# Performance work log

Hardware: AMD Instinct MI355X
Metric: run time of the kernel (lower is better)

Reference implementation:

```python
import jax, jax.numpy as jnp
import numpy as np

N_NODES = 100000
N_EDGES = 1_600_000


def setup_inputs() -> dict:
    key = jax.random.key(0)
    ks = jax.random.split(key, 18)
    glorot = lambda k, fi, fo: jax.random.normal(k, (fi, fo), jnp.float32) * np.sqrt(2.0 / (fi + fo))
    inp = {
        "x": jax.random.normal(ks[0], (N_NODES, 5), jnp.float32),
        "edge_index": jax.random.randint(ks[1], (2, N_EDGES), 0, N_NODES, jnp.int64 if jax.config.jax_enable_x64 else jnp.int32),
        "W1": glorot(ks[2], 5, 32),  "b1": jnp.zeros((32,), jnp.float32),
        "W2": glorot(ks[3], 32, 32), "b2": jnp.zeros((32,), jnp.float32),
        "W3": glorot(ks[4], 32, 32), "b3": jnp.zeros((32,), jnp.float32),
        "Wd": glorot(ks[5], 32, 1),  "bd": jnp.zeros((1,), jnp.float32),
        "Wa": glorot(ks[6], 32, 1),  "ba": jnp.zeros((1,), jnp.float32),
        "Wt": glorot(ks[7], 32, 2),  "bt": jnp.zeros((2,), jnp.float32),
        "Wact": glorot(ks[8], 32, 9), "bact": jnp.zeros((9,), jnp.float32),
    }
    return inp


def _gcn_layer(x, row, col, norm, W, b):
    # GCNConv(add_self_loops=False): out[col] += norm * (x @ W)[row], then + bias
    h = x @ W                                  # [N, F_out]
    msg = h[row] * norm[:, None]               # [E, F_out]
    return jax.ops.segment_sum(msg, col, num_segments=N_NODES) + b


def reference(x, edge_index, W1, b1, W2, b2, W3, b3, Wd, bd, Wa, ba, Wt, bt, Wact, bact):
    row, col = edge_index[0], edge_index[1]
    # symmetric gcn normalization: deg over targets (unit edge weights)
    deg = jax.ops.segment_sum(jnp.ones((row.shape[0],), x.dtype), col, num_segments=N_NODES)
    dis = jnp.where(deg > 0, jax.lax.rsqrt(jnp.maximum(deg, 1.0)), 0.0)
    norm = dis[row] * dis[col]                 # [E]

    h = jax.nn.relu(_gcn_layer(x, row, col, norm, W1, b1))   # dropout = identity (eval)
    h = jax.nn.relu(_gcn_layer(h, row, col, norm, W2, b2))
    h = jax.nn.relu(_gcn_layer(h, row, col, norm, W3, b3))

    distance_scores = (h @ Wd + bd)[:, 0]      # [N]
    attention_scores = (h @ Wa + ba)[:, 0]     # [N]
    target_idx = jnp.argmax(attention_scores)
    h_t = h[target_idx]                        # [32]
    target_location_score = h_t @ Wt + bt      # [2]
    action_logits = h_t @ Wact + bact          # [9]
    return distance_scores, attention_scores, target_location_score, action_logits
```

## Files before the change

kernel.cpp:

```cpp
#include <hip/hip_runtime.h>
#include <hip/hip_fp16.h>
#include <math.h>

#define N_NODES 100000
#define F 32
#define BUCKET 64
#define NB ((N_NODES + BUCKET - 1) / BUCKET)
#define NBLK 128
#define SMAX 1536

__global__ void hist_kernel(const int* __restrict__ col, int* __restrict__ counts, int E) {
    __shared__ int hist[NB];
    int tid = threadIdx.x, blk = blockIdx.x;
    for (int i = tid; i < NB; i += 256) hist[i] = 0;
    __syncthreads();
    int chunk = (E + NBLK - 1) / NBLK;
    int beg = blk * chunk;
    int end = beg + chunk; if (end > E) end = E;
    for (int e = beg + tid; e < end; e += 256) atomicAdd(&hist[col[e] >> 6], 1);
    __syncthreads();
    for (int i = tid; i < NB; i += 256) counts[(size_t)blk * NB + i] = hist[i];
}

__global__ void offA_kernel(const int* __restrict__ counts, int* __restrict__ bucket_base,
                            int* __restrict__ rowstart, int E) {
    __shared__ int tot[NB];
    __shared__ int psum[1024];
    int tid = threadIdx.x;
    for (int b = tid; b < NB; b += 1024) {
        int s = 0;
        for (int blk = 0; blk < NBLK; blk++) s += counts[(size_t)blk * NB + b];
        tot[b] = s;
    }
    __syncthreads();
    int b0 = 2 * tid, b1 = 2 * tid + 1;
    int t0 = (b0 < NB) ? tot[b0] : 0;
    int t1 = (b1 < NB) ? tot[b1] : 0;
    int s = t0 + t1;
    psum[tid] = s;
    __syncthreads();
    for (int off = 1; off < 1024; off <<= 1) {
        int v = (tid >= off) ? psum[tid - off] : 0;
        __syncthreads();
        psum[tid] += v;
        __syncthreads();
    }
    int excl = psum[tid] - s;
    if (b0 < NB) bucket_base[b0] = excl;
    if (b1 < NB) bucket_base[b1] = excl + t0;
    if (tid == 1023) { bucket_base[NB] = psum[1023]; rowstart[N_NODES] = psum[1023]; }
}

__global__ void offB_kernel(const int* __restrict__ counts, const int* __restrict__ bucket_base,
                            int* __restrict__ boff) {
    int b = blockIdx.x * 256 + threadIdx.x;
    if (b >= NB) return;
    int running = bucket_base[b];
    for (int blk = 0; blk < NBLK; blk++) {
        boff[(size_t)blk * NB + b] = running;
        running += counts[(size_t)blk * NB + b];
    }
}

__global__ void scatter_kernel(const int* __restrict__ row, const int* __restrict__ col,
                               const int* __restrict__ boff, unsigned* __restrict__ storage, int E) {
    __shared__ int cur[NB];
    int tid = threadIdx.x, blk = blockIdx.x;
    for (int i = tid; i < NB; i += 256) cur[i] = boff[(size_t)blk * NB + i];
    __syncthreads();
    int chunk = (E + NBLK - 1) / NBLK;
    int beg = blk * chunk;
    int end = beg + chunk; if (end > E) end = E;
    for (int e = beg + tid; e < end; e += 256) {
        int c = col[e], r = row[e];
        int pos = atomicAdd(&cur[c >> 6], 1);
        storage[pos] = ((unsigned)(c & 63) << 17) | (unsigned)r;
    }
}

__global__ void csr_build_kernel(const unsigned* __restrict__ storage, const int* __restrict__ bucket_base,
                                 int* __restrict__ rowstart, int* __restrict__ csr_src,
                                 float* __restrict__ dis, const float* __restrict__ x,
                                 float* __restrict__ xd, int n) {
    __shared__ unsigned sh[SMAX];
    __shared__ int outloc[SMAX];
    __shared__ int hist[BUCKET];
    __shared__ int pre[BUCKET];
    __shared__ int cur[BUCKET];
    __shared__ float dloc[BUCKET];
    int b = blockIdx.x, tid = threadIdx.x;
    if (tid < BUCKET) hist[tid] = 0;
    __syncthreads();
    int base = bucket_base[b];
    int tot = bucket_base[b + 1] - base;
    if (tot > SMAX) tot = SMAX;
    for (int i = tid; i < tot; i += 256) sh[i] = storage[base + i];
    __syncthreads();
    for (int i = tid; i < tot; i += 256) atomicAdd(&hist[sh[i] >> 17], 1);
    __syncthreads();
    if (tid < BUCKET) pre[tid] = hist[tid];
    __syncthreads();
    for (int off = 1; off < BUCKET; off <<= 1) {
        int v = 0;
        if (tid < BUCKET && tid >= off) v = pre[tid - off];
        __syncthreads();
        if (tid < BUCKET && tid >= off) pre[tid] += v;
        __syncthreads();
    }
    if (tid < BUCKET) {
        int excl = pre[tid] - hist[tid];
        cur[tid] = excl;
        int node = b * BUCKET + tid;
        if (node < n) {
            rowstart[node] = base + excl;
            int d = hist[tid];
            float dv = (d > 0) ? rsqrtf((float)d) : 0.0f;
            dis[node] = dv;
            dloc[tid] = dv;
        }
    }
    __syncthreads();
    for (int i = tid; i < BUCKET * 8; i += 256) {
        int nl = i >> 3, f = i & 7;
        int node = b * BUCKET + nl;
        if (node < n) xd[(size_t)node * 8 + f] = (f < 5) ? dloc[nl] * x[(size_t)node * 5 + f] : 0.0f;
    }
    for (int i = tid; i < tot; i += 256) {
        unsigned p = sh[i];
        int pos = atomicAdd(&cur[p >> 17], 1);
        outloc[pos] = (int)(p & 0x1FFFF);
    }
    __syncthreads();
    for (int i = tid; i < tot; i += 256) csr_src[base + i] = outloc[i];
}

__global__ void gather8_kernel(const float* __restrict__ xd, const int* __restrict__ rowstart,
                               const int* __restrict__ csr_src, float* __restrict__ s1, int n) {
    int tid = threadIdx.x;
    int node = blockIdx.x * 32 + (tid >> 3);
    if (node >= n) return;
    int f = tid & 7;
    int start = rowstart[node], end = rowstart[node + 1];
    float a0 = 0, a1 = 0, a2 = 0, a3 = 0, a4 = 0, a5 = 0, a6 = 0, a7 = 0;
    int i = start;
    for (; i + 7 < end; i += 8) {
        int r0 = csr_src[i], r1 = csr_src[i+1], r2 = csr_src[i+2], r3 = csr_src[i+3];
        int r4 = csr_src[i+4], r5 = csr_src[i+5], r6 = csr_src[i+6], r7 = csr_src[i+7];
        a0 += xd[r0*8+f]; a1 += xd[r1*8+f]; a2 += xd[r2*8+f]; a3 += xd[r3*8+f];
        a4 += xd[r4*8+f]; a5 += xd[r5*8+f]; a6 += xd[r6*8+f]; a7 += xd[r7*8+f];
    }
    for (; i < end; i++) a0 += xd[csr_src[i]*8+f];
    s1[node*8+f] = ((a0+a1)+(a2+a3)) + ((a4+a5)+(a6+a7));
}

__global__ void pt1_kernel(const float* __restrict__ s1, const float* __restrict__ dis,
                           const float* __restrict__ W1, const float* __restrict__ b1,
                           __half* __restrict__ gdh, int n) {
    __shared__ float Ws[5 * F];
    int tid = threadIdx.x;
    if (tid < 5 * F) Ws[tid] = W1[tid];
    __syncthreads();
    int node = blockIdx.x * 8 + (tid >> 5);
    if (node >= n) return;
    int f = tid & 31;
    float dv = dis[node];
    float acc = b1[f];
#pragma unroll
    for (int k = 0; k < 5; k++) acc += dv * s1[node*8+k] * Ws[k*F+f];
    float h = acc > 0.0f ? acc : 0.0f;
    gdh[(size_t)node*F+f] = __float2half(dv * h);
}

__global__ void layer_mid_fused(const __half2* __restrict__ gin, const int* __restrict__ rowstart,
                                const int* __restrict__ csr_src, const float* __restrict__ dis,
                                const float* __restrict__ W, const float* __restrict__ bb,
                                __half2* __restrict__ gout, int n) {
    __shared__ float Ws[F * F];
    __shared__ float hs[16][F + 1];
    int tid = threadIdx.x;
    for (int i = tid; i < F * F; i += 256) Ws[i] = W[i];
    int grp = tid >> 4;
    int l2 = tid & 15;
    int node = blockIdx.x * 16 + grp;
    float dv = 0.0f;
    if (node < n) {
        int start = rowstart[node], end = rowstart[node + 1];
        float x0=0,y0=0,x1=0,y1=0,x2=0,y2=0,x3=0,y3=0;
        float x4=0,y4=0,x5=0,y5=0,x6=0,y6=0,x7=0,y7=0;
        int i = start;
        for (; i + 7 < end; i += 8) {
            int r0 = csr_src[i],   r1 = csr_src[i+1], r2 = csr_src[i+2], r3 = csr_src[i+3];
            int r4 = csr_src[i+4], r5 = csr_src[i+5], r6 = csr_src[i+6], r7 = csr_src[i+7];
            float2 f0 = __half22float2(gin[(size_t)r0*16 + l2]);
            float2 f1 = __half22float2(gin[(size_t)r1*16 + l2]);
            float2 f2 = __half22float2(gin[(size_t)r2*16 + l2]);
            float2 f3 = __half22float2(gin[(size_t)r3*16 + l2]);
            float2 f4 = __half22float2(gin[(size_t)r4*16 + l2]);
            float2 f5 = __half22float2(gin[(size_t)r5*16 + l2]);
            float2 f6 = __half22float2(gin[(size_t)r6*16 + l2]);
            float2 f7 = __half22float2(gin[(size_t)r7*16 + l2]);
            x0+=f0.x; y0+=f0.y; x1+=f1.x; y1+=f1.y; x2+=f2.x; y2+=f2.y; x3+=f3.x; y3+=f3.y;
            x4+=f4.x; y4+=f4.y; x5+=f5.x; y5+=f5.y; x6+=f6.x; y6+=f6.y; x7+=f7.x; y7+=f7.y;
        }
        for (; i < end; i++) {
            float2 fv = __half22float2(gin[(size_t)csr_src[i]*16 + l2]);
            x0 += fv.x; y0 += fv.y;
        }
        dv = dis[node];
        hs[grp][2*l2]   = dv * (((x0+x1)+(x2+x3)) + ((x4+x5)+(x6+x7)));
        hs[grp][2*l2+1] = dv * (((y0+y1)+(y2+y3)) + ((y4+y5)+(y6+y7)));
    }
    __syncthreads();
    if (node < n) {
        int fx = 2*l2, fy = 2*l2+1;
        float accx = bb[fx], accy = bb[fy];
#pragma unroll
        for (int k = 0; k < F; k++) {
            float hv = hs[grp][k];
            accx += hv * Ws[k*F+fx];
            accy += hv * Ws[k*F+fy];
        }
        float hx = accx > 0.0f ? accx : 0.0f;
        float hy = accy > 0.0f ? accy : 0.0f;
        gout[(size_t)node*16 + l2] = __floats2half2_rn(dv * hx, dv * hy);
    }
}

__global__ void layer_last_fused(const __half2* __restrict__ gin, const int* __restrict__ rowstart,
                                 const int* __restrict__ csr_src, const float* __restrict__ dis,
                                 const float* __restrict__ W3, const float* __restrict__ b3,
                                 const float* __restrict__ Wd, const float* __restrict__ bd,
                                 const float* __restrict__ Wa, const float* __restrict__ ba,
                                 float* __restrict__ out, float* __restrict__ pmax,
                                 int* __restrict__ pidx, int n) {
    __shared__ float Ws[F * F];
    __shared__ float hs[16][F + 1];
    __shared__ float gmax[16];
    __shared__ int gidx[16];
    int tid = threadIdx.x;
    for (int i = tid; i < F * F; i += 256) Ws[i] = W3[i];
    int grp = tid >> 4;
    int l2 = tid & 15;
    int node = blockIdx.x * 16 + grp;
    float dv = 0.0f;
    if (node < n) {
        int start = rowstart[node], end = rowstart[node + 1];
        float x0=0,y0=0,x1=0,y1=0,x2=0,y2=0,x3=0,y3=0;
        float x4=0,y4=0,x5=0,y5=0,x6=0,y6=0,x7=0,y7=0;
        int i = start;
        for (; i + 7 < end; i += 8) {
            int r0 = csr_src[i],   r1 = csr_src[i+1], r2 = csr_src[i+2], r3 = csr_src[i+3];
            int r4 = csr_src[i+4], r5 = csr_src[i+5], r6 = csr_src[i+6], r7 = csr_src[i+7];
            float2 f0 = __half22float2(gin[(size_t)r0*16 + l2]);
            float2 f1 = __half22float2(gin[(size_t)r1*16 + l2]);
            float2 f2 = __half22float2(gin[(size_t)r2*16 + l2]);
            float2 f3 = __half22float2(gin[(size_t)r3*16 + l2]);
            float2 f4 = __half22float2(gin[(size_t)r4*16 + l2]);
            float2 f5 = __half22float2(gin[(size_t)r5*16 + l2]);
            float2 f6 = __half22float2(gin[(size_t)r6*16 + l2]);
            float2 f7 = __half22float2(gin[(size_t)r7*16 + l2]);
            x0+=f0.x; y0+=f0.y; x1+=f1.x; y1+=f1.y; x2+=f2.x; y2+=f2.y; x3+=f3.x; y3+=f3.y;
            x4+=f4.x; y4+=f4.y; x5+=f5.x; y5+=f5.y; x6+=f6.x; y6+=f6.y; x7+=f7.x; y7+=f7.y;
        }
        for (; i < end; i++) {
            float2 fv = __half22float2(gin[(size_t)csr_src[i]*16 + l2]);
            x0 += fv.x; y0 += fv.y;
        }
        dv = dis[node];
        hs[grp][2*l2]   = dv * (((x0+x1)+(x2+x3)) + ((x4+x5)+(x6+x7)));
        hs[grp][2*l2+1] = dv * (((y0+y1)+(y2+y3)) + ((y4+y5)+(y6+y7)));
    }
    __syncthreads();
    if (node < n) {
        int fx = 2*l2, fy = 2*l2+1;
        float accx = b3[fx], accy = b3[fy];
#pragma unroll
        for (int k = 0; k < F; k++) {
            float hv = hs[grp][k];
            accx += hv * Ws[k*F+fx];
            accy += hv * Ws[k*F+fy];
        }
        float hx = accx > 0.0f ? accx : 0.0f;
        float hy = accy > 0.0f ? accy : 0.0f;
        float dterm = hx * Wd[fx] + hy * Wd[fy];
        float aterm = hx * Wa[fx] + hy * Wa[fy];
#pragma unroll
        for (int off = 8; off > 0; off >>= 1) {
            dterm += __shfl_xor(dterm, off);
            aterm += __shfl_xor(aterm, off);
        }
        if (l2 == 0) {
            out[node] = dterm + bd[0];
            float asc = aterm + ba[0];
            out[N_NODES + node] = asc;
            gmax[grp] = asc;
            gidx[grp] = node;
        }
    } else if (l2 == 0) {
        gmax[grp] = -INFINITY;
        gidx[grp] = 0x7fffffff;
    }
    __syncthreads();
    if (tid == 0) {
        float best = gmax[0]; int bi = gidx[0];
        for (int g = 1; g < 16; g++) {
            if (gmax[g] > best || (gmax[g] == best && gidx[g] < bi)) { best = gmax[g]; bi = gidx[g]; }
        }
        pmax[blockIdx.x] = best;
        pidx[blockIdx.x] = bi;
    }
}

__global__ void final_kernel(const float* __restrict__ pmax, const int* __restrict__ pidx, int nblocks,
                             const __half* __restrict__ gin, const int* __restrict__ rowstart,
                             const int* __restrict__ csr_src, const float* __restrict__ dis,
                             const float* __restrict__ W3, const float* __restrict__ b3,
                             const float* __restrict__ Wt, const float* __restrict__ bt,
                             const float* __restrict__ Wact, const float* __restrict__ bact,
                             float* __restrict__ out) {
    __shared__ float smax[256];
    __shared__ int sidx[256];
    __shared__ float part[8][F];
    __shared__ float hrow[F];
    __shared__ float ht[F];
    int tid = threadIdx.x;
    float best = -INFINITY; int bi = 0x7fffffff;
    for (int i = tid; i < nblocks; i += 256) {
        float v = pmax[i]; int ix = pidx[i];
        if (v > best || (v == best && ix < bi)) { best = v; bi = ix; }
    }
    smax[tid] = best; sidx[tid] = bi;
    __syncthreads();
    for (int st = 128; st > 0; st >>= 1) {
        if (tid < st) {
            float v2 = smax[tid + st]; int i2 = sidx[tid + st];
            if (v2 > smax[tid] || (v2 == smax[tid] && i2 < sidx[tid])) { smax[tid] = v2; sidx[tid] = i2; }
        }
        __syncthreads();
    }
    int target = sidx[0];
    int g = tid >> 5, f = tid & 31;
    int start = rowstart[target], end = rowstart[target + 1];
    float acc = 0.0f;
    for (int i = start + g; i < end; i += 8)
        acc += __half2float(gin[(size_t)csr_src[i] * F + f]);
    part[g][f] = acc;
    __syncthreads();
    if (tid < F) {
        float s = 0.0f;
#pragma unroll
        for (int gg = 0; gg < 8; gg++) s += part[gg][tid];
        hrow[tid] = dis[target] * s;
    }
    __syncthreads();
    if (tid < F) {
        float a = b3[tid];
#pragma unroll
        for (int k = 0; k < F; k++) a += hrow[k] * W3[k*F+tid];
        ht[tid] = a > 0.0f ? a : 0.0f;
    }
    __syncthreads();
    if (tid < 2) {
        float a = bt[tid];
#pragma unroll
        for (int k = 0; k < F; k++) a += ht[k] * Wt[k*2+tid];
        out[2 * N_NODES + tid] = a;
    } else if (tid < 11) {
        int j = tid - 2;
        float a = bact[j];
#pragma unroll
        for (int k = 0; k < F; k++) a += ht[k] * Wact[k*9+j];
        out[2 * N_NODES + 2 + j] = a;
    }
}

extern "C" void kernel_launch(void* const* d_in, const int* in_sizes, int n_in,
                              void* d_out, int out_size, void* d_ws, size_t ws_size,
                              hipStream_t stream) {
    const float* x  = (const float*)d_in[0];
    const int*   ei = (const int*)d_in[1];
    const int E = in_sizes[1] / 2;
    const int* row = ei;
    const int* col = ei + E;
    const float* W1 = (const float*)d_in[2];
    const float* b1 = (const float*)d_in[3];
    const float* W2 = (const float*)d_in[4];
    const float* b2 = (const float*)d_in[5];
    const float* W3 = (const float*)d_in[6];
    const float* b3 = (const float*)d_in[7];
    const float* Wd = (const float*)d_in[8];
    const float* bd = (const float*)d_in[9];
    const float* Wa = (const float*)d_in[10];
    const float* ba = (const float*)d_in[11];
    const float* Wt = (const float*)d_in[12];
    const float* bt = (const float*)d_in[13];
    const float* Wact = (const float*)d_in[14];
    const float* bact = (const float*)d_in[15];

    float* out = (float*)d_out;
    float* ws  = (float*)d_ws;

    float*    dis      = ws;
    float*    xd       = ws + N_NODES;
    float*    s1       = ws + (size_t)9 * N_NODES;
    __half*   gd_a     = (__half*)(ws + (size_t)17 * N_NODES);
    __half*   gd_b     = (__half*)(ws + (size_t)33 * N_NODES);
    unsigned* storage  = (unsigned*)(ws + (size_t)33 * N_NODES);
    int*      bucket_base = (int*)(ws + (size_t)49 * N_NODES);
    int*      counts   = bucket_base + NB + 1;
    int*      boff     = counts + NBLK * NB;
    int*      rowstart = boff + NBLK * NB;
    int*      csr_src  = rowstart + N_NODES + 1;
    float*    pmax     = (float*)(csr_src + E);
    int*      pidx     = (int*)(pmax + 12500);

    const int B = 256;
    const int nb16 = (N_NODES + 15) / 16;

    hist_kernel<<<NBLK, B, 0, stream>>>(col, counts, E);
    offA_kernel<<<1, 1024, 0, stream>>>(counts, bucket_base, rowstart, E);
    offB_kernel<<<(NB + 255) / 256, B, 0, stream>>>(counts, bucket_base, boff);
    scatter_kernel<<<NBLK, B, 0, stream>>>(row, col, boff, storage, E);
    csr_build_kernel<<<NB, B, 0, stream>>>(storage, bucket_base, rowstart, csr_src, dis, x, xd, N_NODES);

    gather8_kernel<<<(N_NODES + 31) / 32, B, 0, stream>>>(xd, rowstart, csr_src, s1, N_NODES);
    pt1_kernel<<<(N_NODES + 7) / 8, B, 0, stream>>>(s1, dis, W1, b1, gd_a, N_NODES);

    layer_mid_fused<<<nb16, B, 0, stream>>>((const __half2*)gd_a, rowstart, csr_src, dis,
                                            W2, b2, (__half2*)gd_b, N_NODES);

    layer_last_fused<<<nb16, B, 0, stream>>>((const __half2*)gd_b, rowstart, csr_src, dis,
                                             W3, b3, Wd, bd, Wa, ba, out, pmax, pidx, N_NODES);
    final_kernel<<<1, B, 0, stream>>>(pmax, pidx, nb16, gd_b, rowstart, csr_src, dis,
                                      W3, b3, Wt, bt, Wact, bact, out);
}
```

Baseline: 279.5 us.

## Fuse layer-1 gather with transform, parallelize bucket totals, deepen gather unroll

Merges the layer-1 neighbour gather and the 5→32 transform into one kernel, so the s1 intermediate is no longer written to and read back from global memory, and one launch is dropped. The per-bucket total reduction moves out of the single-block offset kernel into a multi-block kernel, which removes a serial bottleneck at the cost of one extra launch. The mid and last layer gathers now issue 16 independent index and feature loads per iteration to raise memory-level parallelism, which costs more registers and could lower occupancy.

```diff
diff --git a/kernel.cpp b/kernel.cpp
--- a/kernel.cpp
+++ b/kernel.cpp
@@ -22,17 +22,18 @@
     for (int i = tid; i < NB; i += 256) counts[(size_t)blk * NB + i] = hist[i];
 }
 
-__global__ void offA_kernel(const int* __restrict__ counts, int* __restrict__ bucket_base,
-                            int* __restrict__ rowstart, int E) {
-    __shared__ int tot[NB];
+__global__ void tot_kernel(const int* __restrict__ counts, int* __restrict__ tot) {
+    int b = blockIdx.x * 256 + threadIdx.x;
+    if (b >= NB) return;
+    int s = 0;
+    for (int blk = 0; blk < NBLK; blk++) s += counts[(size_t)blk * NB + b];
+    tot[b] = s;
+}
+
+__global__ void offA_kernel(const int* __restrict__ tot, int* __restrict__ bucket_base,
+                            int* __restrict__ rowstart) {
     __shared__ int psum[1024];
     int tid = threadIdx.x;
-    for (int b = tid; b < NB; b += 1024) {
-        int s = 0;
-        for (int blk = 0; blk < NBLK; blk++) s += counts[(size_t)blk * NB + b];
-        tot[b] = s;
-    }
-    __syncthreads();
     int b0 = 2 * tid, b1 = 2 * tid + 1;
     int t0 = (b0 < NB) ? tot[b0] : 0;
     int t1 = (b1 < NB) ? tot[b1] : 0;
@@ -134,41 +135,46 @@
     for (int i = tid; i < tot; i += 256) csr_src[base + i] = outloc[i];
 }
 
-__global__ void gather8_kernel(const float* __restrict__ xd, const int* __restrict__ rowstart,
-                               const int* __restrict__ csr_src, float* __restrict__ s1, int n) {
-    int tid = threadIdx.x;
-    int node = blockIdx.x * 32 + (tid >> 3);
-    if (node >= n) return;
-    int f = tid & 7;
-    int start = rowstart[node], end = rowstart[node + 1];
-    float a0 = 0, a1 = 0, a2 = 0, a3 = 0, a4 = 0, a5 = 0, a6 = 0, a7 = 0;
-    int i = start;
-    for (; i + 7 < end; i += 8) {
-        int r0 = csr_src[i], r1 = csr_src[i+1], r2 = csr_src[i+2], r3 = csr_src[i+3];
-        int r4 = csr_src[i+4], r5 = csr_src[i+5], r6 = csr_src[i+6], r7 = csr_src[i+7];
-        a0 += xd[r0*8+f]; a1 += xd[r1*8+f]; a2 += xd[r2*8+f]; a3 += xd[r3*8+f];
-        a4 += xd[r4*8+f]; a5 += xd[r5*8+f]; a6 += xd[r6*8+f]; a7 += xd[r7*8+f];
-    }
-    for (; i < end; i++) a0 += xd[csr_src[i]*8+f];
-    s1[node*8+f] = ((a0+a1)+(a2+a3)) + ((a4+a5)+(a6+a7));
-}
-
-__global__ void pt1_kernel(const float* __restrict__ s1, const float* __restrict__ dis,
-                           const float* __restrict__ W1, const float* __restrict__ b1,
-                           __half* __restrict__ gdh, int n) {
+__global__ void layer1_fused(const float* __restrict__ xd, const int* __restrict__ rowstart,
+                             const int* __restrict__ csr_src, const float* __restrict__ dis,
+                             const float* __restrict__ W1, const float* __restrict__ b1,
+                             __half* __restrict__ gda, int n) {
     __shared__ float Ws[5 * F];
+    __shared__ float s1s[32][8];
     int tid = threadIdx.x;
     if (tid < 5 * F) Ws[tid] = W1[tid];
-    __syncthreads();
-    int node = blockIdx.x * 8 + (tid >> 5);
-    if (node >= n) return;
-    int f = tid & 31;
-    float dv = dis[node];
-    float acc = b1[f];
-#pragma unroll
-    for (int k = 0; k < 5; k++) acc += dv * s1[node*8+k] * Ws[k*F+f];
-    float h = acc > 0.0f ? acc : 0.0f;
-    gdh[(size_t)node*F+f] = __float2half(dv * h);
+    int grp = tid >> 3, f = tid & 7;
+    int node = blockIdx.x * 32 + grp;
+    float sum = 0.0f;
+    if (node < n) {
+        int start = rowstart[node], end = rowstart[node + 1];
+        float a0 = 0, a1 = 0, a2 = 0, a3 = 0, a4 = 0, a5 = 0, a6 = 0, a7 = 0;
+        int i = start;
+        for (; i + 7 < end; i += 8) {
+            int r0 = csr_src[i], r1 = csr_src[i+1], r2 = csr_src[i+2], r3 = csr_src[i+3];
+            int r4 = csr_src[i+4], r5 = csr_src[i+5], r6 = csr_src[i+6], r7 = csr_src[i+7];
+            a0 += xd[r0*8+f]; a1 += xd[r1*8+f]; a2 += xd[r2*8+f]; a3 += xd[r3*8+f];
+            a4 += xd[r4*8+f]; a5 += xd[r5*8+f]; a6 += xd[r6*8+f]; a7 += xd[r7*8+f];
+        }
+        for (; i < end; i++) a0 += xd[csr_src[i]*8+f];
+        sum = ((a0+a1)+(a2+a3)) + ((a4+a5)+(a6+a7));
+    }
+    s1s[grp][f] = sum;
+    __syncthreads();
+    if (node < n) {
+        float dv = dis[node];
+        float sk0 = dv * s1s[grp][0], sk1 = dv * s1s[grp][1], sk2 = dv * s1s[grp][2];
+        float sk3 = dv * s1s[grp][3], sk4 = dv * s1s[grp][4];
+        int fb = f * 4;
+#pragma unroll
+        for (int j = 0; j < 4; j++) {
+            int ff = fb + j;
+            float acc = b1[ff] + sk0 * Ws[0*F+ff] + sk1 * Ws[1*F+ff] + sk2 * Ws[2*F+ff]
+                       + sk3 * Ws[3*F+ff] + sk4 * Ws[4*F+ff];
+            float h = acc > 0.0f ? acc : 0.0f;
+            gda[(size_t)node * F + ff] = __float2half(dv * h);
+        }
+    }
 }
 
 __global__ void layer_mid_fused(const __half2* __restrict__ gin, const int* __restrict__ rowstart,
@@ -185,30 +191,41 @@
     float dv = 0.0f;
     if (node < n) {
         int start = rowstart[node], end = rowstart[node + 1];
-        float x0=0,y0=0,x1=0,y1=0,x2=0,y2=0,x3=0,y3=0;
-        float x4=0,y4=0,x5=0,y5=0,x6=0,y6=0,x7=0,y7=0;
+        float accx[4] = {0,0,0,0}, accy[4] = {0,0,0,0};
         int i = start;
+        for (; i + 15 < end; i += 16) {
+            int r[16];
+#pragma unroll
+            for (int j = 0; j < 16; j++) r[j] = csr_src[i + j];
+            __half2 hv[16];
+#pragma unroll
+            for (int j = 0; j < 16; j++) hv[j] = gin[(size_t)r[j] * 16 + l2];
+#pragma unroll
+            for (int j = 0; j < 16; j++) {
+                float2 fv = __half22float2(hv[j]);
+                accx[j & 3] += fv.x; accy[j & 3] += fv.y;
+            }
+        }
         for (; i + 7 < end; i += 8) {
-            int r0 = csr_src[i],   r1 = csr_src[i+1], r2 = csr_src[i+2], r3 = csr_src[i+3];
-            int r4 = csr_src[i+4], r5 = csr_src[i+5], r6 = csr_src[i+6], r7 = csr_src[i+7];
-            float2 f0 = __half22float2(gin[(size_t)r0*16 + l2]);
-            float2 f1 = __half22float2(gin[(size_t)r1*16 + l2]);
-            float2 f2 = __half22float2(gin[(size_t)r2*16 + l2]);
-            float2 f3 = __half22float2(gin[(size_t)r3*16 + l2]);
-            float2 f4 = __half22float2(gin[(size_t)r4*16 + l2]);
-            float2 f5 = __half22float2(gin[(size_t)r5*16 + l2]);
-            float2 f6 = __half22float2(gin[(size_t)r6*16 + l2]);
-            float2 f7 = __half22float2(gin[(size_t)r7*16 + l2]);
-            x0+=f0.x; y0+=f0.y; x1+=f1.x; y1+=f1.y; x2+=f2.x; y2+=f2.y; x3+=f3.x; y3+=f3.y;
-            x4+=f4.x; y4+=f4.y; x5+=f5.x; y5+=f5.y; x6+=f6.x; y6+=f6.y; x7+=f7.x; y7+=f7.y;
+            int r[8];
+#pragma unroll
+            for (int j = 0; j < 8; j++) r[j] = csr_src[i + j];
+            __half2 hv[8];
+#pragma unroll
+            for (int j = 0; j < 8; j++) hv[j] = gin[(size_t)r[j] * 16 + l2];
+#pragma unroll
+            for (int j = 0; j < 8; j++) {
+                float2 fv = __half22float2(hv[j]);
+                accx[j & 3] += fv.x; accy[j & 3] += fv.y;
+            }
         }
         for (; i < end; i++) {
-            float2 fv = __half22float2(gin[(size_t)csr_src[i]*16 + l2]);
-            x0 += fv.x; y0 += fv.y;
+            float2 fv = __half22float2(gin[(size_t)csr_src[i] * 16 + l2]);
+            accx[0] += fv.x; accy[0] += fv.y;
         }
         dv = dis[node];
-        hs[grp][2*l2]   = dv * (((x0+x1)+(x2+x3)) + ((x4+x5)+(x6+x7)));
-        hs[grp][2*l2+1] = dv * (((y0+y1)+(y2+y3)) + ((y4+y5)+(y6+y7)));
+        hs[grp][2*l2]   = dv * ((accx[0]+accx[1]) + (accx[2]+accx[3]));
+        hs[grp][2*l2+1] = dv * ((accy[0]+accy[1]) + (accy[2]+accy[3]));
     }
     __syncthreads();
     if (node < n) {
@@ -245,30 +262,41 @@
     float dv = 0.0f;
     if (node < n) {
         int start = rowstart[node], end = rowstart[node + 1];
-        float x0=0,y0=0,x1=0,y1=0,x2=0,y2=0,x3=0,y3=0;
-        float x4=0,y4=0,x5=0,y5=0,x6=0,y6=0,x7=0,y7=0;
+        float accx[4] = {0,0,0,0}, accy[4] = {0,0,0,0};
         int i = start;
+        for (; i + 15 < end; i += 16) {
+            int r[16];
+#pragma unroll
+            for (int j = 0; j < 16; j++) r[j] = csr_src[i + j];
+            __half2 hv[16];
+#pragma unroll
+            for (int j = 0; j < 16; j++) hv[j] = gin[(size_t)r[j] * 16 + l2];
+#pragma unroll
+            for (int j = 0; j < 16; j++) {
+                float2 fv = __half22float2(hv[j]);
+                accx[j & 3] += fv.x; accy[j & 3] += fv.y;
+            }
+        }
         for (; i + 7 < end; i += 8) {
-            int r0 = csr_src[i],   r1 = csr_src[i+1], r2 = csr_src[i+2], r3 = csr_src[i+3];
-            int r4 = csr_src[i+4], r5 = csr_src[i+5], r6 = csr_src[i+6], r7 = csr_src[i+7];
-            float2 f0 = __half22float2(gin[(size_t)r0*16 + l2]);
-            float2 f1 = __half22float2(gin[(size_t)r1*16 + l2]);
-            float2 f2 = __half22float2(gin[(size_t)r2*16 + l2]);
-            float2 f3 = __half22float2(gin[(size_t)r3*16 + l2]);
-            float2 f4 = __half22float2(gin[(size_t)r4*16 + l2]);
-            float2 f5 = __half22float2(gin[(size_t)r5*16 + l2]);
-            float2 f6 = __half22float2(gin[(size_t)r6*16 + l2]);
-            float2 f7 = __half22float2(gin[(size_t)r7*16 + l2]);
-            x0+=f0.x; y0+=f0.y; x1+=f1.x; y1+=f1.y; x2+=f2.x; y2+=f2.y; x3+=f3.x; y3+=f3.y;
-            x4+=f4.x; y4+=f4.y; x5+=f5.x; y5+=f5.y; x6+=f6.x; y6+=f6.y; x7+=f7.x; y7+=f7.y;
+            int r[8];
+#pragma unroll
+            for (int j = 0; j < 8; j++) r[j] = csr_src[i + j];
+            __half2 hv[8];
+#pragma unroll
+            for (int j = 0; j < 8; j++) hv[j] = gin[(size_t)r[j] * 16 + l2];
+#pragma unroll
+            for (int j = 0; j < 8; j++) {
+                float2 fv = __half22float2(hv[j]);
+                accx[j & 3] += fv.x; accy[j & 3] += fv.y;
+            }
         }
         for (; i < end; i++) {
-            float2 fv = __half22float2(gin[(size_t)csr_src[i]*16 + l2]);
-            x0 += fv.x; y0 += fv.y;
+            float2 fv = __half22float2(gin[(size_t)csr_src[i] * 16 + l2]);
+            accx[0] += fv.x; accy[0] += fv.y;
         }
         dv = dis[node];
-        hs[grp][2*l2]   = dv * (((x0+x1)+(x2+x3)) + ((x4+x5)+(x6+x7)));
-        hs[grp][2*l2+1] = dv * (((y0+y1)+(y2+y3)) + ((y4+y5)+(y6+y7)));
+        hs[grp][2*l2]   = dv * ((accx[0]+accx[1]) + (accx[2]+accx[3]));
+        hs[grp][2*l2+1] = dv * ((accy[0]+accy[1]) + (accy[2]+accy[3]));
     }
     __syncthreads();
     if (node < n) {
@@ -402,7 +430,6 @@
 
     float*    dis      = ws;
     float*    xd       = ws + N_NODES;
-    float*    s1       = ws + (size_t)9 * N_NODES;
     __half*   gd_a     = (__half*)(ws + (size_t)17 * N_NODES);
     __half*   gd_b     = (__half*)(ws + (size_t)33 * N_NODES);
     unsigned* storage  = (unsigned*)(ws + (size_t)33 * N_NODES);
@@ -413,18 +440,19 @@
     int*      csr_src  = rowstart + N_NODES + 1;
     float*    pmax     = (float*)(csr_src + E);
     int*      pidx     = (int*)(pmax + 12500);
+    int*      tot      = pidx + 12500;
 
     const int B = 256;
     const int nb16 = (N_NODES + 15) / 16;
 
     hist_kernel<<<NBLK, B, 0, stream>>>(col, counts, E);
-    offA_kernel<<<1, 1024, 0, stream>>>(counts, bucket_base, rowstart, E);
+    tot_kernel<<<(NB + 255) / 256, B, 0, stream>>>(counts, tot);
+    offA_kernel<<<1, 1024, 0, stream>>>(tot, bucket_base, rowstart);
     offB_kernel<<<(NB + 255) / 256, B, 0, stream>>>(counts, bucket_base, boff);
     scatter_kernel<<<NBLK, B, 0, stream>>>(row, col, boff, storage, E);
     csr_build_kernel<<<NB, B, 0, stream>>>(storage, bucket_base, rowstart, csr_src, dis, x, xd, N_NODES);
 
-    gather8_kernel<<<(N_NODES + 31) / 32, B, 0, stream>>>(xd, rowstart, csr_src, s1, N_NODES);
-    pt1_kernel<<<(N_NODES + 7) / 8, B, 0, stream>>>(s1, dis, W1, b1, gd_a, N_NODES);
+    layer1_fused<<<(N_NODES + 31) / 32, B, 0, stream>>>(xd, rowstart, csr_src, dis, W1, b1, gd_a, N_NODES);
 
     layer_mid_fused<<<nb16, B, 0, stream>>>((const __half2*)gd_a, rowstart, csr_src, dis,
                                             W2, b2, (__half2*)gd_b, N_NODES);
```

New measurement: 262.7 us. 6.0% less time.
